# Optimization experiments

Hardware: AMD Instinct MI355X
Metric: run time of the kernel (lower is better)

The kernel has to match this reference:

```python
import jax, jax.numpy as jnp
import numpy as np


def square_distance(src, dst):
    # src: [B,N,C], dst: [B,M,C] -> [B,N,M] squared euclidean distances
    # ||s||^2 + ||d||^2 - 2 s.d, same expansion as the torch module
    d = -2.0 * jnp.einsum('bnc,bmc->bnm', src, dst)
    d = d + jnp.sum(src * src, axis=-1)[:, :, None]
    d = d + jnp.sum(dst * dst, axis=-1)[:, None, :]
    return d


def setup_inputs() -> dict:
    key = jax.random.key(0)
    k1, k2 = jax.random.split(key)
    B, N, M, C = 32, 4096, 4096, 3
    x = jax.random.normal(k1, (B, N, C), dtype=jnp.float32)
    recon = jax.random.normal(k2, (B, M, C), dtype=jnp.float32)
    return {"x": x, "recon": recon}


def reference(x, recon):
    # Chamfer distance (get_loss). square_distance(recon, x) is the
    # transpose of square_distance(x, recon), so compute once.
    d = square_distance(x, recon)            # [B,N,M]
    cost_p2_p1 = jnp.min(d, axis=-1)         # min over recon for each x point
    cost_p1_p2 = jnp.min(d, axis=-2)         # min over x for each recon point
    loss = jnp.mean(cost_p1_p2) + jnp.mean(cost_p2_p1)
    return loss
```

## Files before the change

kernel.cpp:

```cpp
#include <hip/hip_runtime.h>
#include <float.h>
#include <stdint.h>


typedef short bf16x8 __attribute__((ext_vector_type(8)));
typedef float f32x16 __attribute__((ext_vector_type(16)));

#define BLK 256
#define ONE_BF 0x3F80u

__device__ __forceinline__ uint32_t bf16_rne(float f) {
    uint32_t u = __builtin_bit_cast(uint32_t, f);
    return (u + 0x7FFFu + ((u >> 16) & 1u)) >> 16;
}
__device__ __forceinline__ float bf16f(uint32_t h) {
    return __builtin_bit_cast(float, h << 16);
}

__global__ __launch_bounds__(BLK)
void prep_kernel(const float* __restrict__ x, const float* __restrict__ recon,
                 uint32_t* __restrict__ ws)
{
    int tid = blockIdx.x * BLK + threadIdx.x;
    int arr = tid >> 17;
    int p   = tid & 131071;
    const float* s = arr ? recon : x;
    float a = s[3 * p], b = s[3 * p + 1], c = s[3 * p + 2];
    uint32_t hx = bf16_rne(a), hy = bf16_rne(b), hz = bf16_rne(c);
    uint32_t lx = bf16_rne(a - bf16f(hx));
    uint32_t ly = bf16_rne(b - bf16f(hy));
    uint32_t lz = bf16_rne(c - bf16f(hz));
    float tt = a * a + b * b + c * c;
    uint32_t th = bf16_rne(tt);
    uint32_t tl = bf16_rne(tt - bf16f(th));
    uint4 H0 = make_uint4(hx | (hy << 16), hz | (hx << 16),
                          hy | (hz << 16), lx | (ly << 16));
    uint4 H1 = make_uint4(lz | (th << 16), tl | (lx << 16),
                          ly | (lz << 16), 0u);
    ((uint4*)ws)[tid]          = H0;
    ((uint4*)ws)[262144 + tid] = H1;
}

__global__ __launch_bounds__(BLK, 4)
void chamfer_mfma(const float* __restrict__ x, const float* __restrict__ recon,
                  const uint32_t* __restrict__ ws, float* __restrict__ out,
                  float scale)
{
    const int dir = blockIdx.y;
    const int qb  = blockIdx.x & 15;
    const int b   = blockIdx.x >> 4;
    const float* qsrc = dir ? recon : x;
    const int arrT = dir ? 0 : 1;

    const int tid  = threadIdx.x;
    const int wave = tid >> 6;
    const int lane = tid & 63;
    const int l31  = lane & 31;
    const int lh   = lane >> 5;

    bf16x8 A0, A1;
    {
        int n0 = qb * 256 + wave * 64 + l31;
        #pragma unroll
        for (int rb = 0; rb < 2; ++rb) {
            const float* qp = qsrc + ((size_t)b * 4096 + n0 + rb * 32) * 3;
            float cx = -2.f * qp[0], cy = -2.f * qp[1], cz = -2.f * qp[2];
            uint32_t hx = bf16_rne(cx), hy = bf16_rne(cy), hz = bf16_rne(cz);
            uint32_t lx = bf16_rne(cx - bf16f(hx));
            uint32_t ly = bf16_rne(cy - bf16f(hy));
            uint32_t lz = bf16_rne(cz - bf16f(hz));
            uint32_t w0, w1, w2, w3;
            if (lh == 0) {
                w0 = hx | (hy << 16); w1 = hz | (lx << 16);
                w2 = ly | (lz << 16); w3 = hx | (hy << 16);
            } else {
                w0 = hz | (ONE_BF << 16); w1 = ONE_BF | (lx << 16);
                w2 = ly | (lz << 16);     w3 = 0u;
            }
            union { uint4 u; bf16x8 v; } cvt;
            cvt.u = make_uint4(w0, w1, w2, w3);
            if (rb == 0) A0 = cvt.v; else A1 = cvt.v;
        }
    }

    f32x16 zc = {0,0,0,0,0,0,0,0,0,0,0,0,0,0,0,0};
    float rmn0[16], rmn1[16];
    #pragma unroll
    for (int j = 0; j < 16; ++j) { rmn0[j] = FLT_MAX; rmn1[j] = FLT_MAX; }

    const uint4* rec = (const uint4*)ws
        + (size_t)lh * 262144 + (size_t)arrT * 131072 + (size_t)b * 4096 + l31;

    #pragma unroll 2
    for (int it = 0; it < 128; ++it) {
        union { uint4 u; bf16x8 v; } Bf;
        Bf.u = rec[it * 32];
        f32x16 d0 = __builtin_amdgcn_mfma_f32_32x32x16_bf16(A0, Bf.v, zc, 0, 0, 0);
        f32x16 d1 = __builtin_amdgcn_mfma_f32_32x32x16_bf16(A1, Bf.v, zc, 0, 0, 0);
        #pragma unroll
        for (int j = 0; j < 16; ++j) {
            rmn0[j] = fminf(rmn0[j], d0[j]);
            rmn1[j] = fminf(rmn1[j], d1[j]);
        }
    }

    __shared__ float lmin[256][33];
    #pragma unroll
    for (int j = 0; j < 16; ++j) {
        int rl = (j & 3) + 8 * (j >> 2) + 4 * lh;
        lmin[wave * 64 + rl][l31]      = rmn0[j];
        lmin[wave * 64 + 32 + rl][l31] = rmn1[j];
    }
    __syncthreads();

    float m = lmin[tid][0];
    #pragma unroll
    for (int c = 1; c < 32; ++c) m = fminf(m, lmin[tid][c]);

    const float* qp = qsrc + ((size_t)b * 4096 + qb * 256 + tid) * 3;
    float v = m + qp[0] * qp[0] + qp[1] * qp[1] + qp[2] * qp[2];

    #pragma unroll
    for (int off = 32; off > 0; off >>= 1)
        v += __shfl_down(v, off, 64);
    __shared__ float red[4];
    if (lane == 0) red[wave] = v;
    __syncthreads();
    if (tid == 0)
        atomicAdd(out, (red[0] + red[1] + red[2] + red[3]) * scale);
}

extern "C" void kernel_launch(void* const* d_in, const int* in_sizes, int n_in,
                              void* d_out, int out_size, void* d_ws, size_t ws_size,
                              hipStream_t stream) {
    const float* x     = (const float*)d_in[0];
    const float* recon = (const float*)d_in[1];
    float* out = (float*)d_out;

    const float scale = 1.0f / (32.0f * 4096.0f);

    hipMemsetAsync(out, 0, sizeof(float), stream);

    prep_kernel<<<1024, BLK, 0, stream>>>(x, recon, (uint32_t*)d_ws);

    dim3 g(512, 2);
    chamfer_mfma<<<g, BLK, 0, stream>>>(x, recon, (const uint32_t*)d_ws,
                                        out, scale);
}
```

Measured before the change: 103.6 us.

## Software-pipeline B-tile loads and swizzle block indices for XCD locality

The main MFMA loop now prefetches the next pair of B fragments from the workspace while the current pair is consumed, with four independent MFMAs per iteration and a peeled final iteration. The grid becomes 1D with an index swizzle so that consecutive blocks dispatched to the same XCD work on the same batch and direction, which is meant to improve L2 reuse of the target point array. The prefetch adds register pressure under the 4-wave occupancy bound.

```diff
diff --git a/kernel.cpp b/kernel.cpp
--- a/kernel.cpp
+++ b/kernel.cpp
@@ -46,9 +46,12 @@
                   const uint32_t* __restrict__ ws, float* __restrict__ out,
                   float scale)
 {
-    const int dir = blockIdx.y;
-    const int qb  = blockIdx.x & 15;
-    const int b   = blockIdx.x >> 4;
+    int idx = blockIdx.x;
+    int swz = (idx & 7) * 128 + (idx >> 3);
+    int dir = swz >> 9;
+    int b   = (swz >> 4) & 31;
+    int qb  = swz & 15;
+
     const float* qsrc = dir ? recon : x;
     const int arrT = dir ? 0 : 1;
 
@@ -91,16 +94,35 @@
     const uint4* rec = (const uint4*)ws
         + (size_t)lh * 262144 + (size_t)arrT * 131072 + (size_t)b * 4096 + l31;
 
+    union BU { uint4 u; bf16x8 v; };
+    BU c0, c1, n0v, n1v;
+    c0.u = rec[0]; c1.u = rec[32];
+    const uint4* rp = rec + 64;
+
     #pragma unroll 2
-    for (int it = 0; it < 128; ++it) {
-        union { uint4 u; bf16x8 v; } Bf;
-        Bf.u = rec[it * 32];
-        f32x16 d0 = __builtin_amdgcn_mfma_f32_32x32x16_bf16(A0, Bf.v, zc, 0, 0, 0);
-        f32x16 d1 = __builtin_amdgcn_mfma_f32_32x32x16_bf16(A1, Bf.v, zc, 0, 0, 0);
+    for (int p = 0; p < 63; ++p) {
+        n0v.u = rp[0];
+        n1v.u = rp[32];
+        f32x16 d00 = __builtin_amdgcn_mfma_f32_32x32x16_bf16(A0, c0.v, zc, 0, 0, 0);
+        f32x16 d10 = __builtin_amdgcn_mfma_f32_32x32x16_bf16(A1, c0.v, zc, 0, 0, 0);
+        f32x16 d01 = __builtin_amdgcn_mfma_f32_32x32x16_bf16(A0, c1.v, zc, 0, 0, 0);
+        f32x16 d11 = __builtin_amdgcn_mfma_f32_32x32x16_bf16(A1, c1.v, zc, 0, 0, 0);
         #pragma unroll
         for (int j = 0; j < 16; ++j) {
-            rmn0[j] = fminf(rmn0[j], d0[j]);
-            rmn1[j] = fminf(rmn1[j], d1[j]);
+            rmn0[j] = fminf(rmn0[j], fminf(d00[j], d01[j]));
+            rmn1[j] = fminf(rmn1[j], fminf(d10[j], d11[j]));
+        }
+        c0 = n0v; c1 = n1v; rp += 64;
+    }
+    {
+        f32x16 d00 = __builtin_amdgcn_mfma_f32_32x32x16_bf16(A0, c0.v, zc, 0, 0, 0);
+        f32x16 d10 = __builtin_amdgcn_mfma_f32_32x32x16_bf16(A1, c0.v, zc, 0, 0, 0);
+        f32x16 d01 = __builtin_amdgcn_mfma_f32_32x32x16_bf16(A0, c1.v, zc, 0, 0, 0);
+        f32x16 d11 = __builtin_amdgcn_mfma_f32_32x32x16_bf16(A1, c1.v, zc, 0, 0, 0);
+        #pragma unroll
+        for (int j = 0; j < 16; ++j) {
+            rmn0[j] = fminf(rmn0[j], fminf(d00[j], d01[j]));
+            rmn1[j] = fminf(rmn1[j], fminf(d10[j], d11[j]));
         }
     }
 
@@ -143,7 +165,6 @@
 
     prep_kernel<<<1024, BLK, 0, stream>>>(x, recon, (uint32_t*)d_ws);
 
-    dim3 g(512, 2);
-    chamfer_mfma<<<g, BLK, 0, stream>>>(x, recon, (const uint32_t*)d_ws,
-                                        out, scale);
+    chamfer_mfma<<<1024, BLK, 0, stream>>>(x, recon, (const uint32_t*)d_ws,
+                                           out, scale);
 }
```

Result: slower. 362.0 us (+249.4%).
